# Optimization experiments

Hardware: AMD Instinct MI355X
Metric: run time of the kernel (lower is better)

## Reference

```python
import jax, jax.numpy as jnp
import numpy as np

N, C, E = 4096, 128, 10          # nodes, channels, element types
LMAX = 2
NI = (LMAX + 1) ** 2             # 9 spherical components of node_feats
K = {1: 4, 2: 12, 3: 30}         # number of CG paths per correlation order
DIMS = [2 * L + 1 for L in range(LMAX + 1)]  # output irrep dims [1,3,5]


def setup_inputs() -> dict:
    key = jax.random.key(0)
    ks = iter(jax.random.split(key, 64))
    inp = {}
    inp["node_feats"] = jax.random.normal(next(ks), (N, C, NI), jnp.float32)
    inp["sc"] = jax.random.normal(next(ks), (N, C * sum(DIMS)), jnp.float32)
    z = jax.random.randint(next(ks), (N,), 0, E)
    inp["node_attrs"] = jax.nn.one_hot(z, E, dtype=jnp.float32)
    for L, d in enumerate(DIMS):
        # U tensors: fixed Clebsch-Gordan-structured constants (stand-in values,
        # correct shapes/contraction pattern of MACE's U_matrix buffers).
        inp[f"U3_L{L}"] = jax.random.normal(next(ks), (d, NI, NI, NI, K[3]), jnp.float32) * 0.05
        inp[f"U2_L{L}"] = jax.random.normal(next(ks), (d, NI, NI, K[2]), jnp.float32) * 0.05
        inp[f"U1_L{L}"] = jax.random.normal(next(ks), (d, NI, K[1]), jnp.float32) * 0.05
        # Element-dependent path weights [num_elements, k, channels]
        inp[f"W3_L{L}"] = jax.random.normal(next(ks), (E, K[3], C), jnp.float32) / np.sqrt(K[3])
        inp[f"W2_L{L}"] = jax.random.normal(next(ks), (E, K[2], C), jnp.float32) / np.sqrt(K[2])
        inp[f"W1_L{L}"] = jax.random.normal(next(ks), (E, K[1], C), jnp.float32) / np.sqrt(K[1])
        # o3.Linear channel-mixing weight for this irrep
        inp[f"lin_L{L}"] = jax.random.normal(next(ks), (C, C), jnp.float32)
    return inp


def _contract(x, y, U3, U2, U1, W3, W2, W1):
    """MACE symmetric contraction (correlation=3) for one output irrep.
    x: [b,c,n] node feats, y: [b,e] one-hot element attrs.
    Recursive einsum structure from mace.modules.symmetric_contraction.Contraction."""
    out = jnp.einsum('dijnk,ekc,bcn,be->bcdij', U3, W3, x, y)
    c2 = jnp.einsum('dijk,ekc,be->bcdij', U2, W2, y) + out
    out = jnp.einsum('bcdij,bcj->bcdi', c2, x)
    c1 = jnp.einsum('dik,ekc,be->bcdi', U1, W1, y) + out
    return jnp.einsum('bcdi,bci->bcd', c1, x)  # [b,c,d]


def reference(node_feats, sc, node_attrs,
              U3_L0, U2_L0, U1_L0, W3_L0, W2_L0, W1_L0, lin_L0,
              U3_L1, U2_L1, U1_L1, W3_L1, W2_L1, W1_L1, lin_L1,
              U3_L2, U2_L2, U1_L2, W3_L2, W2_L2, W1_L2, lin_L2):
    Us = [(U3_L0, U2_L0, U1_L0), (U3_L1, U2_L1, U1_L1), (U3_L2, U2_L2, U1_L2)]
    Ws = [(W3_L0, W2_L0, W1_L0), (W3_L1, W2_L1, W1_L1), (W3_L2, W2_L2, W1_L2)]
    lins = [lin_L0, lin_L1, lin_L2]
    c = node_feats.shape[1]
    norm = jnp.asarray(1.0 / np.sqrt(c), node_feats.dtype)
    outs = []
    for (u3, u2, u1), (w3, w2, w1), lw in zip(Us, Ws, lins):
        o = _contract(node_feats, node_attrs, u3, u2, u1, w3, w2, w1)  # [b,c,d]
        o = jnp.einsum('bcd,cf->bfd', o, lw) * norm                    # o3.Linear mix
        outs.append(o.reshape(o.shape[0], -1))
    return jnp.concatenate(outs, axis=-1) + sc
```

## Files before the change

kernel.cpp:

```cpp
#include <hip/hip_runtime.h>

#define NNODES 4096
#define NCH    128
#define NE     10
#define PADN   4736
#define NCHUNK 74
#define TSTRIDE 2048
#define DGSTRIDE 672


struct MTab { unsigned short v[220]; };
static constexpr MTab make_mtab() {
    MTab t{};
    int m = 0;
    for (int i = 0; i < 9; ++i) {
        t.v[m++] = (unsigned short)((1 << 12) | (i << 8) | (i << 4) | i);
        for (int j = i; j < 9; ++j) {
            t.v[m++] = (unsigned short)((2 << 12) | (i << 8) | (j << 4) | j);
            for (int n = j; n < 9; ++n)
                t.v[m++] = (unsigned short)((3 << 12) | (i << 8) | (j << 4) | n);
        }
    }
    return t;
}
__constant__ MTab c_mtab = make_mtab();

__global__ __launch_bounds__(1024) void k_prep(
    const float* __restrict__ attrs,
    const float* __restrict__ U3_0, const float* __restrict__ U3_1, const float* __restrict__ U3_2,
    const float* __restrict__ W3_0, const float* __restrict__ W3_1, const float* __restrict__ W3_2,
    const float* __restrict__ U2_0, const float* __restrict__ U2_1, const float* __restrict__ U2_2,
    const float* __restrict__ W2_0, const float* __restrict__ W2_1, const float* __restrict__ W2_2,
    const float* __restrict__ U1_0, const float* __restrict__ U1_1, const float* __restrict__ U1_2,
    const float* __restrict__ W1_0, const float* __restrict__ W1_1, const float* __restrict__ W1_2,
    int* __restrict__ list, int* __restrict__ chunkinfo,
    float* __restrict__ wcat, float* __restrict__ Usym)
{
    int bid = blockIdx.x, t = threadIdx.x;
    if (bid == 0) {
        __shared__ int cnt[64][NE];
        __shared__ int pfx[64][NE];
        __shared__ int tot[NE];
        __shared__ int base[NE + 1], cbase[NE + 1];
        int w = t >> 6, lane = t & 63;
        unsigned long long lmask = (1ull << lane) - 1ull;
        int mye[4];
#pragma unroll
        for (int k = 0; k < 4; ++k) {
            int b = k * 1024 + t;
            const float* y = attrs + (size_t)b * NE;
            int e = 0;
#pragma unroll
            for (int u = 0; u < NE; ++u) if (y[u] > 0.5f) e = u;
            mye[k] = e;
#pragma unroll
            for (int u = 0; u < NE; ++u) {
                unsigned long long mb = __ballot(e == u);
                if (lane == 0) cnt[w * 4 + k][u] = __popcll(mb);
            }
        }
        for (int i = t; i < PADN; i += 1024) list[i] = -1;
        __syncthreads();
        if (t < 640) {
            int e = t >> 6, wi = t & 63;
            int v = cnt[wi][e];
            int inc = v;
#pragma unroll
            for (int d = 1; d < 64; d <<= 1) {
                int o = __shfl_up(inc, d, 64);
                if (wi >= d) inc += o;
            }
            pfx[wi][e] = inc - v;
            if (wi == 63) tot[e] = inc;
        }
        __syncthreads();
        if (t == 0) {
            int off = 0, goff = 0;
            for (int e = 0; e < NE; ++e) {
                base[e] = off; cbase[e] = goff;
                int nc = (tot[e] + 63) >> 6;
                off += nc * 64; goff += nc;
            }
            base[NE] = off; cbase[NE] = goff;
        }
        __syncthreads();
        if (t < 80) {
            int info = -1;
            if (t < cbase[NE]) {
                int e = 0;
                while (!(t >= cbase[e] && t < cbase[e + 1])) ++e;
                int k = t - cbase[e];
                int valid = tot[e] - k * 64; if (valid > 64) valid = 64;
                info = (base[e] + k * 64) | (valid << 16) | (e << 24);
            }
            chunkinfo[t] = info;
        } else if (t < 91) {
            chunkinfo[t] = cbase[t - 80];
        }
#pragma unroll
        for (int k = 0; k < 4; ++k) {
            int e = mye[k];
#pragma unroll
            for (int u = 0; u < NE; ++u) {
                unsigned long long mb = __ballot(e == u);
                if (e == u) {
                    int pos = base[u] + pfx[w * 4 + k][u] + __popcll(mb & lmask);
                    list[pos] = k * 1024 + t;
                }
            }
        }
    } else if (bid <= 10) {
        int e = bid - 1;
#pragma unroll 1
        for (int L = 0; L < 3; ++L) {
            const float* W1 = (L == 0) ? W1_0 : (L == 1) ? W1_1 : W1_2;
            const float* W2 = (L == 0) ? W2_0 : (L == 1) ? W2_1 : W2_2;
            const float* W3 = (L == 0) ? W3_0 : (L == 1) ? W3_1 : W3_2;
            for (int it = t; it < 48 * 128; it += 1024) {
                int c = it & 127, k = it >> 7;
                float v = 0.0f;
                if (k < 4)       v = W1[((size_t)e * 4 + k) * 128 + c];
                else if (k < 16) v = W2[((size_t)e * 12 + (k - 4)) * 128 + c];
                else if (k < 46) v = W3[((size_t)e * 30 + (k - 16)) * 128 + c];
                wcat[(((size_t)L * NE + e) * 48 + k) * 128 + c] = v;
            }
        }
    } else {
        int D = bid - 11;
        const float *U3, *U2, *U1; int dloc;
        if (D == 0)      { U3 = U3_0; U2 = U2_0; U1 = U1_0; dloc = 0; }
        else if (D < 4)  { U3 = U3_1; U2 = U2_1; U1 = U1_1; dloc = D - 1; }
        else             { U3 = U3_2; U2 = U2_2; U1 = U1_2; dloc = D - 4; }
        for (int it = t; it < 219 * 48; it += 1024) {
            int m = it / 48, k = it - m * 48;
            unsigned mv = c_mtab.v[m];
            int kind = mv >> 12, i = (mv >> 8) & 15, j = (mv >> 4) & 15, n = mv & 15;
            float v = 0.0f;
            if (kind == 1) {
                if (k < 4) v = U1[(size_t)(dloc * 9 + i) * 4 + k];
            } else if (kind == 2) {
                if (k >= 4 && k < 16) {
                    int kk = k - 4;
                    v = U2[(size_t)(dloc * 81 + i * 9 + j) * 12 + kk];
                    if (i != j) v += U2[(size_t)(dloc * 81 + j * 9 + i) * 12 + kk];
                }
            } else {
                if (k >= 16 && k < 46) {
                    int kk = k - 16;
                    v = U3[((size_t)dloc * 729 + i * 81 + j * 9 + n) * 30 + kk];
                    if (i == j) {
                        if (j != n)
                            v += U3[((size_t)dloc * 729 + i * 81 + n * 9 + i) * 30 + kk]
                               + U3[((size_t)dloc * 729 + n * 81 + i * 9 + i) * 30 + kk];
                    } else if (j == n) {
                        v += U3[((size_t)dloc * 729 + j * 81 + i * 9 + j) * 30 + kk]
                           + U3[((size_t)dloc * 729 + j * 81 + j * 9 + i) * 30 + kk];
                    } else {
                        v += U3[((size_t)dloc * 729 + i * 81 + n * 9 + j) * 30 + kk]
                           + U3[((size_t)dloc * 729 + j * 81 + i * 9 + n) * 30 + kk]
                           + U3[((size_t)dloc * 729 + j * 81 + n * 9 + i) * 30 + kk]
                           + U3[((size_t)dloc * 729 + n * 81 + i * 9 + j) * 30 + kk]
                           + U3[((size_t)dloc * 729 + n * 81 + j * 9 + i) * 30 + kk];
                    }
                }
            }
            Usym[((size_t)D * 219 + m) * 48 + k] = v;
        }
    }
}

__global__ __launch_bounds__(256) void k_tab(
    const float* __restrict__ wcat, const float* __restrict__ Usym,
    float* __restrict__ Sws)
{
    __shared__ __align__(16) float tile[84 * 129];
    int bid = blockIdx.x;
    int e = bid / 24, r0 = bid - e * 24;
    int dg = r0 >> 3, mh = r0 & 7;
    int m0 = mh * 28, m1 = m0 + 28; if (m1 > 219) m1 = 219;
    int t = threadIdx.x;
    int c = t & 127;
    int sub = __builtin_amdgcn_readfirstlane(t >> 7);
    int D0 = dg * 3;
    int LA = (D0 == 0) ? 0 : (D0 < 4 ? 1 : 2);
    int LB = (D0 + 1 < 4) ? 1 : 2;

    float wcA[48], wcB[48];
#pragma unroll
    for (int k = 0; k < 48; ++k) {
        wcA[k] = wcat[(((size_t)LA * NE + e) * 48 + k) * 128 + c];
        wcB[k] = wcat[(((size_t)LB * NE + e) * 48 + k) * 128 + c];
    }

#pragma unroll 1
    for (int m = m0 + sub; m < m1; m += 2) {
        unsigned mv = c_mtab.v[m];
        int kind = mv >> 12;
        const float* up0 = Usym + ((size_t)D0 * 219 + m) * 48;
        const float* up1 = up0 + 219 * 48;
        const float* up2 = up1 + 219 * 48;
        float a0 = 0.0f, a1 = 0.0f, a2 = 0.0f;
        if (kind == 1) {
#pragma unroll
            for (int k = 0; k < 4; ++k) {
                a0 = fmaf(up0[k], wcA[k], a0);
                a1 = fmaf(up1[k], wcB[k], a1);
                a2 = fmaf(up2[k], wcB[k], a2);
            }
        } else if (kind == 2) {
#pragma unroll
            for (int k = 4; k < 16; ++k) {
                a0 = fmaf(up0[k], wcA[k], a0);
                a1 = fmaf(up1[k], wcB[k], a1);
                a2 = fmaf(up2[k], wcB[k], a2);
            }
        } else {
#pragma unroll
            for (int k = 16; k < 46; ++k) {
                a0 = fmaf(up0[k], wcA[k], a0);
                a1 = fmaf(up1[k], wcB[k], a1);
                a2 = fmaf(up2[k], wcB[k], a2);
            }
        }
        int rr = (m - m0) * 3;
        tile[(rr + 0) * 129 + c] = a0;
        tile[(rr + 1) * 129 + c] = a1;
        tile[(rr + 2) * 129 + c] = a2;
    }
    __syncthreads();

    int w = t >> 6, lane = t & 63;
    int nrows = (m1 - m0) * 3;
#pragma unroll 1
    for (int cc = 0; cc < 32; ++cc) {
        int co = w * 32 + cc;
        float* op = Sws + ((size_t)e * NCH + co) * TSTRIDE + dg * DGSTRIDE + m0 * 3;
#pragma unroll
        for (int rr = lane; rr < 84; rr += 64)
            if (rr < nrows) op[rr] = tile[rr * 129 + co];
    }
}

template <int NB>
__device__ __forceinline__ void do_chunks(
    const float* __restrict__ tab, const float* __restrict__ nf,
    const int* __restrict__ list, const int* __restrict__ chunkinfo,
    float* __restrict__ prep, int c, int gi, int lane)
{
    int pos[NB];
    float x[NB][9];
#pragma unroll
    for (int u = 0; u < NB; ++u) {
        int info = __builtin_amdgcn_readfirstlane(chunkinfo[gi + u]);
        pos[u] = (info & 0xffff) + lane;
        int b = list[pos[u]];
        const float* xp = nf + ((size_t)(b < 0 ? 0 : b) * 128 + c) * 9;
#pragma unroll
        for (int n = 0; n < 9; ++n) x[u][n] = (b >= 0) ? xp[n] : 0.0f;
    }

#pragma unroll 1
    for (int dg = 0; dg < 3; ++dg) {
        const float* s = tab + dg * DGSTRIDE;
        float a3[NB][3];
#pragma unroll
        for (int u = 0; u < NB; ++u)
#pragma unroll
            for (int d = 0; d < 3; ++d) a3[u][d] = 0.0f;
        int p = 0;
#pragma unroll
        for (int i = 0; i < 9; ++i) {
            float a2[NB][3];
#pragma unroll
            for (int d = 0; d < 3; ++d) {
                float tv = s[p + d];
#pragma unroll
                for (int u = 0; u < NB; ++u) a2[u][d] = tv;
            }
            p += 3;
#pragma unroll
            for (int j = i; j < 9; ++j) {
                float a1[NB][3];
#pragma unroll
                for (int d = 0; d < 3; ++d) {
                    float tv = s[p + d];
#pragma unroll
                    for (int u = 0; u < NB; ++u) a1[u][d] = tv;
                }
                p += 3;
#pragma unroll
                for (int n = j; n < 9; ++n) {
#pragma unroll
                    for (int d = 0; d < 3; ++d) {
                        float tv = s[p + d];
#pragma unroll
                        for (int u = 0; u < NB; ++u)
                            a1[u][d] = fmaf(tv, x[u][n], a1[u][d]);
                    }
                    p += 3;
                }
#pragma unroll
                for (int u = 0; u < NB; ++u)
#pragma unroll
                    for (int d = 0; d < 3; ++d)
                        a2[u][d] = fmaf(a1[u][d], x[u][j], a2[u][d]);
            }
#pragma unroll
            for (int u = 0; u < NB; ++u)
#pragma unroll
                for (int d = 0; d < 3; ++d)
                    a3[u][d] = fmaf(a2[u][d], x[u][i], a3[u][d]);
        }
#pragma unroll
        for (int u = 0; u < NB; ++u)
#pragma unroll
            for (int d = 0; d < 3; ++d)
                prep[(size_t)(dg * 3 + d) * PADN + pos[u]] = a3[u][d];
    }
}

__global__ __launch_bounds__(256) void k_main(
    const float* __restrict__ nf, const int* __restrict__ list,
    const int* __restrict__ chunkinfo, const float* __restrict__ Sws,
    float* __restrict__ pre)
{
    __shared__ __align__(16) float tab[TSTRIDE];
    int c = blockIdx.x, e = blockIdx.y;
    int t = threadIdx.x;
    int w = t >> 6, lane = t & 63;
    int cb0 = chunkinfo[80 + e], cb1 = chunkinfo[81 + e];
    if (cb0 >= cb1) return;

    {
        const float4* src = (const float4*)(Sws + ((size_t)e * NCH + c) * TSTRIDE);
        float4* dst = (float4*)tab;
        dst[t] = src[t];
        dst[t + 256] = src[t + 256];
    }
    __syncthreads();

    float* prep = pre + (size_t)c * 9 * PADN;

#pragma unroll 1
    for (int gi = cb0 + 2 * w; gi < cb1; gi += 8) {
        if (gi + 1 < cb1)
            do_chunks<2>(tab, nf, list, chunkinfo, prep, c, gi, lane);
        else
            do_chunks<1>(tab, nf, list, chunkinfo, prep, c, gi, lane);
    }
}

__global__ __launch_bounds__(256) void k_mix(
    const float* __restrict__ pre, const int* __restrict__ chunkinfo,
    const float* __restrict__ lin0, const float* __restrict__ lin1,
    const float* __restrict__ lin2, float* __restrict__ mixed)
{
    __shared__ __align__(16) float pt[128 * 64];
    int bid = blockIdx.x;
    int nt = bid >> 1;
    int fbase = (bid & 1) * 64;
    int n0 = nt * 64;
    int D = nt / NCHUNK;
    int g = nt - D * NCHUNK;
    if (chunkinfo[g] == -1) return;
    const float* lin = (D == 0) ? lin0 : (D < 4 ? lin1 : lin2);
    int t = threadIdx.x;

    {
        int q4 = (t & 15) * 4;
        int cb = t >> 4;
#pragma unroll
        for (int k = 0; k < 8; ++k) {
            int c = cb + k * 16;
            float4 v = *(const float4*)&pre[(size_t)c * 9 * PADN + n0 + q4];
            *(float4*)&pt[c * 64 + q4] = v;
        }
    }
    __syncthreads();

    int tq = t & 63;
    int f0 = fbase + __builtin_amdgcn_readfirstlane(t >> 6) * 16;
    float acc[16];
#pragma unroll
    for (int f = 0; f < 16; ++f) acc[f] = 0.0f;

#pragma unroll 4
    for (int c = 0; c < 128; ++c) {
        float pv = pt[c * 64 + tq];
        const float* lr = lin + c * 128 + f0;
#pragma unroll
        for (int f = 0; f < 16; ++f)
            acc[f] = fmaf(pv, lr[f], acc[f]);
    }

    const float nrm = 0.08838834764831845f;
#pragma unroll
    for (int f = 0; f < 16; ++f)
        mixed[(size_t)(f0 + f) * 9 * PADN + n0 + tq] = acc[f] * nrm;
}

__global__ __launch_bounds__(256) void k_out(
    const float* __restrict__ mixed, const int* __restrict__ list,
    const int* __restrict__ chunkinfo, const float* __restrict__ sc,
    float* __restrict__ out)
{
    __shared__ float tr[64 * 73];
    int fc = blockIdx.x, g = blockIdx.y;
    if (chunkinfo[g] == -1) return;
    int t = threadIdx.x;
    int fbase = fc * 8;
    int tf = t >> 6, tq = t & 63;

#pragma unroll
    for (int k = 0; k < 18; ++k) {
        int row = k * 4 + tf;
        int f = row / 9, D = row - f * 9;
        float v = mixed[((size_t)(fbase + f) * 9 + D) * PADN + g * 64 + tq];
        tr[tq * 73 + row] = v;
    }
    __syncthreads();

#pragma unroll 1
    for (int k = 0; k < 18; ++k) {
        int idx = k * 256 + t;
        int node = idx / 72, col = idx - node * 72;
        int b = list[g * 64 + node];
        if (b < 0) continue;
        int row, gcol;
        if (col < 8)       { row = col * 9;                       gcol = fbase + col; }
        else if (col < 32) { int u = col - 8;  int f = u / 3, dl = u - f * 3;
                             row = f * 9 + 1 + dl;                gcol = 128 + fbase * 3 + u; }
        else               { int u = col - 32; int f = u / 5, dl = u - f * 5;
                             row = f * 9 + 4 + dl;                gcol = 512 + fbase * 5 + u; }
        out[(size_t)b * 1152 + gcol] = tr[node * 73 + row] + sc[(size_t)b * 1152 + gcol];
    }
}

extern "C" void kernel_launch(void* const* d_in, const int* in_sizes, int n_in,
                              void* d_out, int out_size, void* d_ws, size_t ws_size,
                              hipStream_t stream)
{
    const float* nf    = (const float*)d_in[0];
    const float* sc    = (const float*)d_in[1];
    const float* attrs = (const float*)d_in[2];
    const float *U3s[3], *U2s[3], *U1s[3], *W3s[3], *W2s[3], *W1s[3], *lins[3];
    for (int L = 0; L < 3; ++L) {
        const int o = 3 + 7 * L;
        U3s[L]  = (const float*)d_in[o + 0];
        U2s[L]  = (const float*)d_in[o + 1];
        U1s[L]  = (const float*)d_in[o + 2];
        W3s[L]  = (const float*)d_in[o + 3];
        W2s[L]  = (const float*)d_in[o + 4];
        W1s[L]  = (const float*)d_in[o + 5];
        lins[L] = (const float*)d_in[o + 6];
    }

    float* wsf     = (float*)d_ws;
    int* chunkinfo = (int*)d_ws;
    int* list      = chunkinfo + 96;
    float* Sws   = wsf + 4864;
    float* pre   = Sws + (size_t)NE * NCH * TSTRIDE;
    float* mixed = pre + (size_t)NCH * 9 * PADN;
    float* wcat  = mixed + (size_t)NCH * 9 * PADN;
    float* Usym  = wcat + (size_t)3 * NE * 48 * 128;

    k_prep<<<20, 1024, 0, stream>>>(attrs,
                                    U3s[0], U3s[1], U3s[2], W3s[0], W3s[1], W3s[2],
                                    U2s[0], U2s[1], U2s[2], W2s[0], W2s[1], W2s[2],
                                    U1s[0], U1s[1], U1s[2], W1s[0], W1s[1], W1s[2],
                                    list, chunkinfo, wcat, Usym);
    k_tab<<<240, 256, 0, stream>>>(wcat, Usym, Sws);
    k_main<<<dim3(128, 10), 256, 0, stream>>>(nf, list, chunkinfo, Sws, pre);
    k_mix<<<1332, 256, 0, stream>>>(pre, chunkinfo, lins[0], lins[1], lins[2], mixed);
    k_out<<<dim3(16, NCHUNK), 256, 0, stream>>>(mixed, list, chunkinfo, sc, (float*)d_out);
}
```

Before: 241.7 us.

## Fuse prep and table kernels into one launch; widen k_mix per-thread outputs

Merges k_prep and k_tab into a single k_pre kernel. Block 0 builds the element lists with 256 threads, and the other 240 blocks compute their symmetrized U slice into shared memory and read W directly, so the wcat/Usym global intermediates and one kernel launch go away. U symmetrization work is now duplicated across the 10 element blocks. k_mix also computes 32 output features per thread instead of 16, halving its grid to improve reuse of the staged tile, at the cost of more registers per thread.

```diff
diff --git a/kernel.cpp b/kernel.cpp
--- a/kernel.cpp
+++ b/kernel.cpp
@@ -25,7 +25,7 @@
 }
 __constant__ MTab c_mtab = make_mtab();
 
-__global__ __launch_bounds__(1024) void k_prep(
+__global__ __launch_bounds__(256) void k_pre(
     const float* __restrict__ attrs,
     const float* __restrict__ U3_0, const float* __restrict__ U3_1, const float* __restrict__ U3_2,
     const float* __restrict__ W3_0, const float* __restrict__ W3_1, const float* __restrict__ W3_2,
@@ -33,21 +33,24 @@
     const float* __restrict__ W2_0, const float* __restrict__ W2_1, const float* __restrict__ W2_2,
     const float* __restrict__ U1_0, const float* __restrict__ U1_1, const float* __restrict__ U1_2,
     const float* __restrict__ W1_0, const float* __restrict__ W1_1, const float* __restrict__ W1_2,
-    int* __restrict__ list, int* __restrict__ chunkinfo,
-    float* __restrict__ wcat, float* __restrict__ Usym)
-{
+    int* __restrict__ list, int* __restrict__ chunkinfo, float* __restrict__ Sws)
+{
+    __shared__ __align__(16) float smem[84 * 129 + 3 * 28 * 48];
     int bid = blockIdx.x, t = threadIdx.x;
+    int w = t >> 6, lane = t & 63;
+
     if (bid == 0) {
-        __shared__ int cnt[64][NE];
-        __shared__ int pfx[64][NE];
-        __shared__ int tot[NE];
-        __shared__ int base[NE + 1], cbase[NE + 1];
-        int w = t >> 6, lane = t & 63;
+        int* ib = (int*)smem;
+        int (*cnt)[NE] = (int(*)[NE])ib;
+        int (*pfx)[NE] = (int(*)[NE])(ib + 640);
+        int* tot   = ib + 1280;
+        int* base  = ib + 1296;
+        int* cbase = ib + 1312;
         unsigned long long lmask = (1ull << lane) - 1ull;
-        int mye[4];
-#pragma unroll
-        for (int k = 0; k < 4; ++k) {
-            int b = k * 1024 + t;
+        int mye[16];
+#pragma unroll
+        for (int k = 0; k < 16; ++k) {
+            int b = k * 256 + t;
             const float* y = attrs + (size_t)b * NE;
             int e = 0;
 #pragma unroll
@@ -56,22 +59,22 @@
 #pragma unroll
             for (int u = 0; u < NE; ++u) {
                 unsigned long long mb = __ballot(e == u);
-                if (lane == 0) cnt[w * 4 + k][u] = __popcll(mb);
-            }
-        }
-        for (int i = t; i < PADN; i += 1024) list[i] = -1;
+                if (lane == 0) cnt[w * 16 + k][u] = __popcll(mb);
+            }
+        }
+        for (int i = t; i < PADN; i += 256) list[i] = -1;
         __syncthreads();
-        if (t < 640) {
-            int e = t >> 6, wi = t & 63;
-            int v = cnt[wi][e];
+#pragma unroll 1
+        for (int e = w; e < NE; e += 4) {
+            int v = cnt[lane][e];
             int inc = v;
 #pragma unroll
             for (int d = 1; d < 64; d <<= 1) {
                 int o = __shfl_up(inc, d, 64);
-                if (wi >= d) inc += o;
-            }
-            pfx[wi][e] = inc - v;
-            if (wi == 63) tot[e] = inc;
+                if (lane >= d) inc += o;
+            }
+            pfx[lane][e] = inc - v;
+            if (lane == 63) tot[e] = inc;
         }
         __syncthreads();
         if (t == 0) {
@@ -98,44 +101,44 @@
             chunkinfo[t] = cbase[t - 80];
         }
 #pragma unroll
-        for (int k = 0; k < 4; ++k) {
+        for (int k = 0; k < 16; ++k) {
             int e = mye[k];
 #pragma unroll
             for (int u = 0; u < NE; ++u) {
                 unsigned long long mb = __ballot(e == u);
                 if (e == u) {
-                    int pos = base[u] + pfx[w * 4 + k][u] + __popcll(mb & lmask);
-                    list[pos] = k * 1024 + t;
+                    int pos = base[u] + pfx[w * 16 + k][u] + __popcll(mb & lmask);
+                    list[pos] = k * 256 + t;
                 }
             }
         }
-    } else if (bid <= 10) {
-        int e = bid - 1;
-#pragma unroll 1
-        for (int L = 0; L < 3; ++L) {
-            const float* W1 = (L == 0) ? W1_0 : (L == 1) ? W1_1 : W1_2;
-            const float* W2 = (L == 0) ? W2_0 : (L == 1) ? W2_1 : W2_2;
-            const float* W3 = (L == 0) ? W3_0 : (L == 1) ? W3_1 : W3_2;
-            for (int it = t; it < 48 * 128; it += 1024) {
-                int c = it & 127, k = it >> 7;
-                float v = 0.0f;
-                if (k < 4)       v = W1[((size_t)e * 4 + k) * 128 + c];
-                else if (k < 16) v = W2[((size_t)e * 12 + (k - 4)) * 128 + c];
-                else if (k < 46) v = W3[((size_t)e * 30 + (k - 16)) * 128 + c];
-                wcat[(((size_t)L * NE + e) * 48 + k) * 128 + c] = v;
-            }
-        }
-    } else {
-        int D = bid - 11;
-        const float *U3, *U2, *U1; int dloc;
-        if (D == 0)      { U3 = U3_0; U2 = U2_0; U1 = U1_0; dloc = 0; }
-        else if (D < 4)  { U3 = U3_1; U2 = U2_1; U1 = U1_1; dloc = D - 1; }
-        else             { U3 = U3_2; U2 = U2_2; U1 = U1_2; dloc = D - 4; }
-        for (int it = t; it < 219 * 48; it += 1024) {
-            int m = it / 48, k = it - m * 48;
+        return;
+    }
+
+    float* tile = smem;
+    float* us   = smem + 84 * 129;
+    int r = bid - 1;
+    int e = r / 24, r0 = r - e * 24;
+    int dg = r0 >> 3, mh = r0 & 7;
+    int m0 = mh * 28, m1 = m0 + 28; if (m1 > 219) m1 = 219;
+    int D0 = dg * 3;
+    int LA = (D0 == 0) ? 0 : (D0 < 4 ? 1 : 2);
+    int LB = (D0 + 1 < 4) ? 1 : 2;
+
+#pragma unroll 1
+    for (int it = t; it < 3 * 28 * 48; it += 256) {
+        int k = it % 48, rest = it / 48;
+        int mm = rest % 28, dr = rest / 28;
+        int m = m0 + mm;
+        float v = 0.0f;
+        if (m < 219) {
+            int D = D0 + dr;
+            const float *U3, *U2, *U1; int dloc;
+            if (D == 0)      { U3 = U3_0; U2 = U2_0; U1 = U1_0; dloc = 0; }
+            else if (D < 4)  { U3 = U3_1; U2 = U2_1; U1 = U1_1; dloc = D - 1; }
+            else             { U3 = U3_2; U2 = U2_2; U1 = U1_2; dloc = D - 4; }
             unsigned mv = c_mtab.v[m];
             int kind = mv >> 12, i = (mv >> 8) & 15, j = (mv >> 4) & 15, n = mv & 15;
-            float v = 0.0f;
             if (kind == 1) {
                 if (k < 4) v = U1[(size_t)(dloc * 9 + i) * 4 + k];
             } else if (kind == 2) {
@@ -164,41 +167,37 @@
                     }
                 }
             }
-            Usym[((size_t)D * 219 + m) * 48 + k] = v;
-        }
-    }
-}
-
-__global__ __launch_bounds__(256) void k_tab(
-    const float* __restrict__ wcat, const float* __restrict__ Usym,
-    float* __restrict__ Sws)
-{
-    __shared__ __align__(16) float tile[84 * 129];
-    int bid = blockIdx.x;
-    int e = bid / 24, r0 = bid - e * 24;
-    int dg = r0 >> 3, mh = r0 & 7;
-    int m0 = mh * 28, m1 = m0 + 28; if (m1 > 219) m1 = 219;
-    int t = threadIdx.x;
+        }
+        us[it] = v;
+    }
+
     int c = t & 127;
     int sub = __builtin_amdgcn_readfirstlane(t >> 7);
-    int D0 = dg * 3;
-    int LA = (D0 == 0) ? 0 : (D0 < 4 ? 1 : 2);
-    int LB = (D0 + 1 < 4) ? 1 : 2;
-
+    const float* W1a = (LA == 0) ? W1_0 : (LA == 1) ? W1_1 : W1_2;
+    const float* W2a = (LA == 0) ? W2_0 : (LA == 1) ? W2_1 : W2_2;
+    const float* W3a = (LA == 0) ? W3_0 : (LA == 1) ? W3_1 : W3_2;
+    const float* W1b = (LB == 1) ? W1_1 : W1_2;
+    const float* W2b = (LB == 1) ? W2_1 : W2_2;
+    const float* W3b = (LB == 1) ? W3_1 : W3_2;
     float wcA[48], wcB[48];
 #pragma unroll
     for (int k = 0; k < 48; ++k) {
-        wcA[k] = wcat[(((size_t)LA * NE + e) * 48 + k) * 128 + c];
-        wcB[k] = wcat[(((size_t)LB * NE + e) * 48 + k) * 128 + c];
-    }
+        float a, b;
+        if (k < 4)       { a = W1a[((size_t)e * 4 + k) * 128 + c];        b = W1b[((size_t)e * 4 + k) * 128 + c]; }
+        else if (k < 16) { a = W2a[((size_t)e * 12 + (k - 4)) * 128 + c]; b = W2b[((size_t)e * 12 + (k - 4)) * 128 + c]; }
+        else if (k < 46) { a = W3a[((size_t)e * 30 + (k - 16)) * 128 + c]; b = W3b[((size_t)e * 30 + (k - 16)) * 128 + c]; }
+        else             { a = 0.0f; b = 0.0f; }
+        wcA[k] = a; wcB[k] = b;
+    }
+    __syncthreads();
 
 #pragma unroll 1
     for (int m = m0 + sub; m < m1; m += 2) {
         unsigned mv = c_mtab.v[m];
         int kind = mv >> 12;
-        const float* up0 = Usym + ((size_t)D0 * 219 + m) * 48;
-        const float* up1 = up0 + 219 * 48;
-        const float* up2 = up1 + 219 * 48;
+        const float* up0 = us + (0 * 28 + (m - m0)) * 48;
+        const float* up1 = us + (1 * 28 + (m - m0)) * 48;
+        const float* up2 = us + (2 * 28 + (m - m0)) * 48;
         float a0 = 0.0f, a1 = 0.0f, a2 = 0.0f;
         if (kind == 1) {
 #pragma unroll
@@ -229,7 +228,6 @@
     }
     __syncthreads();
 
-    int w = t >> 6, lane = t & 63;
     int nrows = (m1 - m0) * 3;
 #pragma unroll 1
     for (int cc = 0; cc < 32; ++cc) {
@@ -356,9 +354,7 @@
     const float* __restrict__ lin2, float* __restrict__ mixed)
 {
     __shared__ __align__(16) float pt[128 * 64];
-    int bid = blockIdx.x;
-    int nt = bid >> 1;
-    int fbase = (bid & 1) * 64;
+    int nt = blockIdx.x;
     int n0 = nt * 64;
     int D = nt / NCHUNK;
     int g = nt - D * NCHUNK;
@@ -379,23 +375,23 @@
     __syncthreads();
 
     int tq = t & 63;
-    int f0 = fbase + __builtin_amdgcn_readfirstlane(t >> 6) * 16;
-    float acc[16];
-#pragma unroll
-    for (int f = 0; f < 16; ++f) acc[f] = 0.0f;
-
-#pragma unroll 4
+    int f0 = __builtin_amdgcn_readfirstlane(t >> 6) * 32;
+    float acc[32];
+#pragma unroll
+    for (int f = 0; f < 32; ++f) acc[f] = 0.0f;
+
+#pragma unroll 2
     for (int c = 0; c < 128; ++c) {
         float pv = pt[c * 64 + tq];
         const float* lr = lin + c * 128 + f0;
 #pragma unroll
-        for (int f = 0; f < 16; ++f)
+        for (int f = 0; f < 32; ++f)
             acc[f] = fmaf(pv, lr[f], acc[f]);
     }
 
     const float nrm = 0.08838834764831845f;
 #pragma unroll
-    for (int f = 0; f < 16; ++f)
+    for (int f = 0; f < 32; ++f)
         mixed[(size_t)(f0 + f) * 9 * PADN + n0 + tq] = acc[f] * nrm;
 }
 
@@ -461,16 +457,13 @@
     float* Sws   = wsf + 4864;
     float* pre   = Sws + (size_t)NE * NCH * TSTRIDE;
     float* mixed = pre + (size_t)NCH * 9 * PADN;
-    float* wcat  = mixed + (size_t)NCH * 9 * PADN;
-    float* Usym  = wcat + (size_t)3 * NE * 48 * 128;
-
-    k_prep<<<20, 1024, 0, stream>>>(attrs,
-                                    U3s[0], U3s[1], U3s[2], W3s[0], W3s[1], W3s[2],
-                                    U2s[0], U2s[1], U2s[2], W2s[0], W2s[1], W2s[2],
-                                    U1s[0], U1s[1], U1s[2], W1s[0], W1s[1], W1s[2],
-                                    list, chunkinfo, wcat, Usym);
-    k_tab<<<240, 256, 0, stream>>>(wcat, Usym, Sws);
+
+    k_pre<<<241, 256, 0, stream>>>(attrs,
+                                   U3s[0], U3s[1], U3s[2], W3s[0], W3s[1], W3s[2],
+                                   U2s[0], U2s[1], U2s[2], W2s[0], W2s[1], W2s[2],
+                                   U1s[0], U1s[1], U1s[2], W1s[0], W1s[1], W1s[2],
+                                   list, chunkinfo, Sws);
     k_main<<<dim3(128, 10), 256, 0, stream>>>(nf, list, chunkinfo, Sws, pre);
-    k_mix<<<1332, 256, 0, stream>>>(pre, chunkinfo, lins[0], lins[1], lins[2], mixed);
+    k_mix<<<666, 256, 0, stream>>>(pre, chunkinfo, lins[0], lins[1], lins[2], mixed);
     k_out<<<dim3(16, NCHUNK), 256, 0, stream>>>(mixed, list, chunkinfo, sc, (float*)d_out);
 }
```

Result: no change. 244.4 us (+1.1%).

## Split k_main work into per-irrep-group units and move node bucketing into k_tab

Applied to the files above, without the earlier changes.

The node-by-element bucketing pass moves out of the 1024-thread k_prep into an extra block of k_tab, using 256 threads and reusing the shared tile, so k_prep only builds weight and U tables. In k_main, the work is no longer split per chunk pair with all three irrep groups done serially in one wave. Each (chunk pair, irrep group) becomes a unit spread across the four waves, which improves load balance when an element has few chunks. Node features are reloaded only when the chunk pair changes. The trade-off is that k_tab's critical path now includes the serial bucketing block, and more node-feature reloads can occur.

```diff
diff --git a/kernel.cpp b/kernel.cpp
--- a/kernel.cpp
+++ b/kernel.cpp
@@ -26,91 +26,17 @@
 __constant__ MTab c_mtab = make_mtab();
 
 __global__ __launch_bounds__(1024) void k_prep(
-    const float* __restrict__ attrs,
     const float* __restrict__ U3_0, const float* __restrict__ U3_1, const float* __restrict__ U3_2,
     const float* __restrict__ W3_0, const float* __restrict__ W3_1, const float* __restrict__ W3_2,
     const float* __restrict__ U2_0, const float* __restrict__ U2_1, const float* __restrict__ U2_2,
     const float* __restrict__ W2_0, const float* __restrict__ W2_1, const float* __restrict__ W2_2,
     const float* __restrict__ U1_0, const float* __restrict__ U1_1, const float* __restrict__ U1_2,
     const float* __restrict__ W1_0, const float* __restrict__ W1_1, const float* __restrict__ W1_2,
-    int* __restrict__ list, int* __restrict__ chunkinfo,
     float* __restrict__ wcat, float* __restrict__ Usym)
 {
     int bid = blockIdx.x, t = threadIdx.x;
-    if (bid == 0) {
-        __shared__ int cnt[64][NE];
-        __shared__ int pfx[64][NE];
-        __shared__ int tot[NE];
-        __shared__ int base[NE + 1], cbase[NE + 1];
-        int w = t >> 6, lane = t & 63;
-        unsigned long long lmask = (1ull << lane) - 1ull;
-        int mye[4];
-#pragma unroll
-        for (int k = 0; k < 4; ++k) {
-            int b = k * 1024 + t;
-            const float* y = attrs + (size_t)b * NE;
-            int e = 0;
-#pragma unroll
-            for (int u = 0; u < NE; ++u) if (y[u] > 0.5f) e = u;
-            mye[k] = e;
-#pragma unroll
-            for (int u = 0; u < NE; ++u) {
-                unsigned long long mb = __ballot(e == u);
-                if (lane == 0) cnt[w * 4 + k][u] = __popcll(mb);
-            }
-        }
-        for (int i = t; i < PADN; i += 1024) list[i] = -1;
-        __syncthreads();
-        if (t < 640) {
-            int e = t >> 6, wi = t & 63;
-            int v = cnt[wi][e];
-            int inc = v;
-#pragma unroll
-            for (int d = 1; d < 64; d <<= 1) {
-                int o = __shfl_up(inc, d, 64);
-                if (wi >= d) inc += o;
-            }
-            pfx[wi][e] = inc - v;
-            if (wi == 63) tot[e] = inc;
-        }
-        __syncthreads();
-        if (t == 0) {
-            int off = 0, goff = 0;
-            for (int e = 0; e < NE; ++e) {
-                base[e] = off; cbase[e] = goff;
-                int nc = (tot[e] + 63) >> 6;
-                off += nc * 64; goff += nc;
-            }
-            base[NE] = off; cbase[NE] = goff;
-        }
-        __syncthreads();
-        if (t < 80) {
-            int info = -1;
-            if (t < cbase[NE]) {
-                int e = 0;
-                while (!(t >= cbase[e] && t < cbase[e + 1])) ++e;
-                int k = t - cbase[e];
-                int valid = tot[e] - k * 64; if (valid > 64) valid = 64;
-                info = (base[e] + k * 64) | (valid << 16) | (e << 24);
-            }
-            chunkinfo[t] = info;
-        } else if (t < 91) {
-            chunkinfo[t] = cbase[t - 80];
-        }
-#pragma unroll
-        for (int k = 0; k < 4; ++k) {
-            int e = mye[k];
-#pragma unroll
-            for (int u = 0; u < NE; ++u) {
-                unsigned long long mb = __ballot(e == u);
-                if (e == u) {
-                    int pos = base[u] + pfx[w * 4 + k][u] + __popcll(mb & lmask);
-                    list[pos] = k * 1024 + t;
-                }
-            }
-        }
-    } else if (bid <= 10) {
-        int e = bid - 1;
+    if (bid < 10) {
+        int e = bid;
 #pragma unroll 1
         for (int L = 0; L < 3; ++L) {
             const float* W1 = (L == 0) ? W1_0 : (L == 1) ? W1_1 : W1_2;
@@ -126,7 +52,7 @@
             }
         }
     } else {
-        int D = bid - 11;
+        int D = bid - 10;
         const float *U3, *U2, *U1; int dloc;
         if (D == 0)      { U3 = U3_0; U2 = U2_0; U1 = U1_0; dloc = 0; }
         else if (D < 4)  { U3 = U3_1; U2 = U2_1; U1 = U1_1; dloc = D - 1; }
@@ -170,15 +96,94 @@
 }
 
 __global__ __launch_bounds__(256) void k_tab(
+    const float* __restrict__ attrs,
     const float* __restrict__ wcat, const float* __restrict__ Usym,
-    float* __restrict__ Sws)
+    int* __restrict__ list, int* __restrict__ chunkinfo, float* __restrict__ Sws)
 {
     __shared__ __align__(16) float tile[84 * 129];
-    int bid = blockIdx.x;
-    int e = bid / 24, r0 = bid - e * 24;
+    int bid = blockIdx.x, t = threadIdx.x;
+    int w = t >> 6, lane = t & 63;
+
+    if (bid == 0) {
+        int* ib = (int*)tile;
+        int (*cnt)[NE] = (int(*)[NE])ib;
+        int (*pfx)[NE] = (int(*)[NE])(ib + 640);
+        int* tot   = ib + 1280;
+        int* base  = ib + 1296;
+        int* cbase = ib + 1312;
+        unsigned long long lmask = (1ull << lane) - 1ull;
+        int mye[16];
+#pragma unroll
+        for (int k = 0; k < 16; ++k) {
+            int b = k * 256 + t;
+            const float* y = attrs + (size_t)b * NE;
+            int e = 0;
+#pragma unroll
+            for (int u = 0; u < NE; ++u) if (y[u] > 0.5f) e = u;
+            mye[k] = e;
+#pragma unroll
+            for (int u = 0; u < NE; ++u) {
+                unsigned long long mb = __ballot(e == u);
+                if (lane == 0) cnt[w * 16 + k][u] = __popcll(mb);
+            }
+        }
+        for (int i = t; i < PADN; i += 256) list[i] = -1;
+        __syncthreads();
+#pragma unroll 1
+        for (int e = w; e < NE; e += 4) {
+            int v = cnt[lane][e];
+            int inc = v;
+#pragma unroll
+            for (int d = 1; d < 64; d <<= 1) {
+                int o = __shfl_up(inc, d, 64);
+                if (lane >= d) inc += o;
+            }
+            pfx[lane][e] = inc - v;
+            if (lane == 63) tot[e] = inc;
+        }
+        __syncthreads();
+        if (t == 0) {
+            int off = 0, goff = 0;
+            for (int e = 0; e < NE; ++e) {
+                base[e] = off; cbase[e] = goff;
+                int nc = (tot[e] + 63) >> 6;
+                off += nc * 64; goff += nc;
+            }
+            base[NE] = off; cbase[NE] = goff;
+        }
+        __syncthreads();
+        if (t < 80) {
+            int info = -1;
+            if (t < cbase[NE]) {
+                int e = 0;
+                while (!(t >= cbase[e] && t < cbase[e + 1])) ++e;
+                int k = t - cbase[e];
+                int valid = tot[e] - k * 64; if (valid > 64) valid = 64;
+                info = (base[e] + k * 64) | (valid << 16) | (e << 24);
+            }
+            chunkinfo[t] = info;
+        } else if (t < 91) {
+            chunkinfo[t] = cbase[t - 80];
+        }
+#pragma unroll
+        for (int k = 0; k < 16; ++k) {
+            int e = mye[k];
+#pragma unroll
+            for (int u = 0; u < NE; ++u) {
+                unsigned long long mb = __ballot(e == u);
+                if (e == u) {
+                    int pos = base[u] + pfx[w * 16 + k][u] + __popcll(mb & lmask);
+                    list[pos] = k * 256 + t;
+                }
+            }
+        }
+        return;
+    }
+
+    int r = bid - 1;
+    int e = r / 24, r0 = r - e * 24;
     int dg = r0 >> 3, mh = r0 & 7;
     int m0 = mh * 28, m1 = m0 + 28; if (m1 > 219) m1 = 219;
-    int t = threadIdx.x;
     int c = t & 127;
     int sub = __builtin_amdgcn_readfirstlane(t >> 7);
     int D0 = dg * 3;
@@ -229,7 +234,6 @@
     }
     __syncthreads();
 
-    int w = t >> 6, lane = t & 63;
     int nrows = (m1 - m0) * 3;
 #pragma unroll 1
     for (int cc = 0; cc < 32; ++cc) {
@@ -242,81 +246,64 @@
 }
 
 template <int NB>
-__device__ __forceinline__ void do_chunks(
-    const float* __restrict__ tab, const float* __restrict__ nf,
-    const int* __restrict__ list, const int* __restrict__ chunkinfo,
-    float* __restrict__ prep, int c, int gi, int lane)
-{
-    int pos[NB];
-    float x[NB][9];
-#pragma unroll
-    for (int u = 0; u < NB; ++u) {
-        int info = __builtin_amdgcn_readfirstlane(chunkinfo[gi + u]);
-        pos[u] = (info & 0xffff) + lane;
-        int b = list[pos[u]];
-        const float* xp = nf + ((size_t)(b < 0 ? 0 : b) * 128 + c) * 9;
-#pragma unroll
-        for (int n = 0; n < 9; ++n) x[u][n] = (b >= 0) ? xp[n] : 0.0f;
-    }
-
-#pragma unroll 1
-    for (int dg = 0; dg < 3; ++dg) {
-        const float* s = tab + dg * DGSTRIDE;
-        float a3[NB][3];
-#pragma unroll
-        for (int u = 0; u < NB; ++u)
-#pragma unroll
-            for (int d = 0; d < 3; ++d) a3[u][d] = 0.0f;
-        int p = 0;
-#pragma unroll
-        for (int i = 0; i < 9; ++i) {
-            float a2[NB][3];
+__device__ __forceinline__ void do_unit(
+    const float* __restrict__ s, float* __restrict__ prep,
+    int dbase, const float (&x)[2][9], const int (&pos)[2])
+{
+    float a3[NB][3];
+#pragma unroll
+    for (int u = 0; u < NB; ++u)
+#pragma unroll
+        for (int d = 0; d < 3; ++d) a3[u][d] = 0.0f;
+    int p = 0;
+#pragma unroll
+    for (int i = 0; i < 9; ++i) {
+        float a2[NB][3];
+#pragma unroll
+        for (int d = 0; d < 3; ++d) {
+            float tv = s[p + d];
+#pragma unroll
+            for (int u = 0; u < NB; ++u) a2[u][d] = tv;
+        }
+        p += 3;
+#pragma unroll
+        for (int j = i; j < 9; ++j) {
+            float a1[NB][3];
 #pragma unroll
             for (int d = 0; d < 3; ++d) {
                 float tv = s[p + d];
 #pragma unroll
-                for (int u = 0; u < NB; ++u) a2[u][d] = tv;
+                for (int u = 0; u < NB; ++u) a1[u][d] = tv;
             }
             p += 3;
 #pragma unroll
-            for (int j = i; j < 9; ++j) {
-                float a1[NB][3];
+            for (int n = j; n < 9; ++n) {
 #pragma unroll
                 for (int d = 0; d < 3; ++d) {
                     float tv = s[p + d];
 #pragma unroll
-                    for (int u = 0; u < NB; ++u) a1[u][d] = tv;
+                    for (int u = 0; u < NB; ++u)
+                        a1[u][d] = fmaf(tv, x[u][n], a1[u][d]);
                 }
                 p += 3;
-#pragma unroll
-                for (int n = j; n < 9; ++n) {
-#pragma unroll
-                    for (int d = 0; d < 3; ++d) {
-                        float tv = s[p + d];
-#pragma unroll
-                        for (int u = 0; u < NB; ++u)
-                            a1[u][d] = fmaf(tv, x[u][n], a1[u][d]);
-                    }
-                    p += 3;
-                }
-#pragma unroll
-                for (int u = 0; u < NB; ++u)
-#pragma unroll
-                    for (int d = 0; d < 3; ++d)
-                        a2[u][d] = fmaf(a1[u][d], x[u][j], a2[u][d]);
             }
 #pragma unroll
             for (int u = 0; u < NB; ++u)
 #pragma unroll
                 for (int d = 0; d < 3; ++d)
-                    a3[u][d] = fmaf(a2[u][d], x[u][i], a3[u][d]);
+                    a2[u][d] = fmaf(a1[u][d], x[u][j], a2[u][d]);
         }
 #pragma unroll
         for (int u = 0; u < NB; ++u)
 #pragma unroll
             for (int d = 0; d < 3; ++d)
-                prep[(size_t)(dg * 3 + d) * PADN + pos[u]] = a3[u][d];
-    }
+                a3[u][d] = fmaf(a2[u][d], x[u][i], a3[u][d]);
+    }
+#pragma unroll
+    for (int u = 0; u < NB; ++u)
+#pragma unroll
+        for (int d = 0; d < 3; ++d)
+            prep[(size_t)(dbase + d) * PADN + pos[u]] = a3[u][d];
 }
 
 __global__ __launch_bounds__(256) void k_main(
@@ -339,14 +326,37 @@
     }
     __syncthreads();
 
+    int nch = cb1 - cb0;
+    int ncp = (nch + 1) >> 1;
+    int nunits = ncp * 3;
     float* prep = pre + (size_t)c * 9 * PADN;
 
-#pragma unroll 1
-    for (int gi = cb0 + 2 * w; gi < cb1; gi += 8) {
-        if (gi + 1 < cb1)
-            do_chunks<2>(tab, nf, list, chunkinfo, prep, c, gi, lane);
-        else
-            do_chunks<1>(tab, nf, list, chunkinfo, prep, c, gi, lane);
+    float x[2][9];
+    int pos[2];
+    int prev_cp = -1, nb = 0;
+#pragma unroll 1
+    for (int u = w; u < nunits; u += 4) {
+        int dg = u / ncp;
+        int cp = u - dg * ncp;
+        if (cp != prev_cp) {
+            prev_cp = cp;
+            int gi = cb0 + cp * 2;
+            nb = (gi + 1 < cb1) ? 2 : 1;
+#pragma unroll
+            for (int uu = 0; uu < 2; ++uu) {
+                if (uu < nb) {
+                    int info = __builtin_amdgcn_readfirstlane(chunkinfo[gi + uu]);
+                    pos[uu] = (info & 0xffff) + lane;
+                    int b = list[pos[uu]];
+                    const float* xp = nf + ((size_t)(b < 0 ? 0 : b) * 128 + c) * 9;
+#pragma unroll
+                    for (int n = 0; n < 9; ++n) x[uu][n] = (b >= 0) ? xp[n] : 0.0f;
+                }
+            }
+        }
+        const float* s = tab + dg * DGSTRIDE;
+        if (nb == 2) do_unit<2>(s, prep, dg * 3, x, pos);
+        else         do_unit<1>(s, prep, dg * 3, x, pos);
     }
 }
 
@@ -464,12 +474,11 @@
     float* wcat  = mixed + (size_t)NCH * 9 * PADN;
     float* Usym  = wcat + (size_t)3 * NE * 48 * 128;
 
-    k_prep<<<20, 1024, 0, stream>>>(attrs,
-                                    U3s[0], U3s[1], U3s[2], W3s[0], W3s[1], W3s[2],
+    k_prep<<<19, 1024, 0, stream>>>(U3s[0], U3s[1], U3s[2], W3s[0], W3s[1], W3s[2],
                                     U2s[0], U2s[1], U2s[2], W2s[0], W2s[1], W2s[2],
                                     U1s[0], U1s[1], U1s[2], W1s[0], W1s[1], W1s[2],
-                                    list, chunkinfo, wcat, Usym);
-    k_tab<<<240, 256, 0, stream>>>(wcat, Usym, Sws);
+                                    wcat, Usym);
+    k_tab<<<241, 256, 0, stream>>>(attrs, wcat, Usym, list, chunkinfo, Sws);
     k_main<<<dim3(128, 10), 256, 0, stream>>>(nf, list, chunkinfo, Sws, pre);
     k_mix<<<1332, 256, 0, stream>>>(pre, chunkinfo, lins[0], lins[1], lins[2], mixed);
     k_out<<<dim3(16, NCHUNK), 256, 0, stream>>>(mixed, list, chunkinfo, sc, (float*)d_out);
```

After: 296.6 us. +22.7%, slower.

## Split k_main into one 64-thread block per chunk pair for load balance

Applied to the files above, without the earlier changes.

k_main used to launch one 256-thread block per (channel, element), with four waves striding over that element's chunk pairs, so the work per block was uneven. It now launches one single-wave block per (channel, chunk pair), using a per-element pair prefix sum that k_prep adds to chunkinfo. The goal is to spread work evenly across CUs and raise occupancy. The cost is that each block reloads the 8KB table from Sws, and the grid is padded to 42 pairs, with surplus blocks exiting early.

```diff
diff --git a/kernel.cpp b/kernel.cpp
--- a/kernel.cpp
+++ b/kernel.cpp
@@ -41,7 +41,7 @@
         __shared__ int cnt[64][NE];
         __shared__ int pfx[64][NE];
         __shared__ int tot[NE];
-        __shared__ int base[NE + 1], cbase[NE + 1];
+        __shared__ int base[NE + 1], cbase[NE + 1], pb[NE + 1];
         int w = t >> 6, lane = t & 63;
         unsigned long long lmask = (1ull << lane) - 1ull;
         int mye[4];
@@ -75,13 +75,13 @@
         }
         __syncthreads();
         if (t == 0) {
-            int off = 0, goff = 0;
+            int off = 0, goff = 0, pp = 0;
             for (int e = 0; e < NE; ++e) {
-                base[e] = off; cbase[e] = goff;
+                base[e] = off; cbase[e] = goff; pb[e] = pp;
                 int nc = (tot[e] + 63) >> 6;
-                off += nc * 64; goff += nc;
-            }
-            base[NE] = off; cbase[NE] = goff;
+                off += nc * 64; goff += nc; pp += (nc + 1) >> 1;
+            }
+            base[NE] = off; cbase[NE] = goff; pb[NE] = pp;
         }
         __syncthreads();
         if (t < 80) {
@@ -96,6 +96,8 @@
             chunkinfo[t] = info;
         } else if (t < 91) {
             chunkinfo[t] = cbase[t - 80];
+        } else if (t < 102) {
+            chunkinfo[t] = pb[t - 91];
         }
 #pragma unroll
         for (int k = 0; k < 4; ++k) {
@@ -319,35 +321,34 @@
     }
 }
 
-__global__ __launch_bounds__(256) void k_main(
+__global__ __launch_bounds__(64) void k_main(
     const float* __restrict__ nf, const int* __restrict__ list,
     const int* __restrict__ chunkinfo, const float* __restrict__ Sws,
     float* __restrict__ pre)
 {
     __shared__ __align__(16) float tab[TSTRIDE];
-    int c = blockIdx.x, e = blockIdx.y;
-    int t = threadIdx.x;
-    int w = t >> 6, lane = t & 63;
+    int c = blockIdx.x, p = blockIdx.y;
+    int lane = threadIdx.x;
+    if (p >= chunkinfo[101]) return;
+    int e = 0;
+#pragma unroll
+    for (int u = 1; u < NE; ++u) e += (p >= chunkinfo[91 + u]) ? 1 : 0;
+    int lp = p - chunkinfo[91 + e];
     int cb0 = chunkinfo[80 + e], cb1 = chunkinfo[81 + e];
-    if (cb0 >= cb1) return;
+    int gi = cb0 + 2 * lp;
 
     {
         const float4* src = (const float4*)(Sws + ((size_t)e * NCH + c) * TSTRIDE);
         float4* dst = (float4*)tab;
-        dst[t] = src[t];
-        dst[t + 256] = src[t + 256];
+#pragma unroll
+        for (int k = 0; k < 8; ++k)
+            dst[lane + 64 * k] = src[lane + 64 * k];
     }
     __syncthreads();
 
     float* prep = pre + (size_t)c * 9 * PADN;
-
-#pragma unroll 1
-    for (int gi = cb0 + 2 * w; gi < cb1; gi += 8) {
-        if (gi + 1 < cb1)
-            do_chunks<2>(tab, nf, list, chunkinfo, prep, c, gi, lane);
-        else
-            do_chunks<1>(tab, nf, list, chunkinfo, prep, c, gi, lane);
-    }
+    if (gi + 1 < cb1) do_chunks<2>(tab, nf, list, chunkinfo, prep, c, gi, lane);
+    else              do_chunks<1>(tab, nf, list, chunkinfo, prep, c, gi, lane);
 }
 
 __global__ __launch_bounds__(256) void k_mix(
@@ -457,7 +458,7 @@
 
     float* wsf     = (float*)d_ws;
     int* chunkinfo = (int*)d_ws;
-    int* list      = chunkinfo + 96;
+    int* list      = chunkinfo + 112;
     float* Sws   = wsf + 4864;
     float* pre   = Sws + (size_t)NE * NCH * TSTRIDE;
     float* mixed = pre + (size_t)NCH * 9 * PADN;
@@ -470,7 +471,7 @@
                                     U1s[0], U1s[1], U1s[2], W1s[0], W1s[1], W1s[2],
                                     list, chunkinfo, wcat, Usym);
     k_tab<<<240, 256, 0, stream>>>(wcat, Usym, Sws);
-    k_main<<<dim3(128, 10), 256, 0, stream>>>(nf, list, chunkinfo, Sws, pre);
+    k_main<<<dim3(128, 42), 64, 0, stream>>>(nf, list, chunkinfo, Sws, pre);
     k_mix<<<1332, 256, 0, stream>>>(pre, chunkinfo, lins[0], lins[1], lins[2], mixed);
     k_out<<<dim3(16, NCHUNK), 256, 0, stream>>>(mixed, list, chunkinfo, sc, (float*)d_out);
 }
```

Result: no change. 245.3 us (+1.5%).
